# Kernel tuning notes

Measured on AMD Instinct MI355X. Metric: run time of the kernel, lower is better.

Reference implementation:

```python
import jax, jax.numpy as jnp
import numpy as np

EPS = 1e-5

def _layernorm(x, w, b):
    mu = jnp.mean(x, axis=-1, keepdims=True)
    var = jnp.mean(jnp.square(x - mu), axis=-1, keepdims=True)
    return (x - mu) * jax.lax.rsqrt(var + EPS) * w + b

def setup_inputs() -> dict:
    N, C = 768, 128
    key = jax.random.key(0)
    ks = jax.random.split(key, 5)
    s = 0.02
    return {
        "pair": jax.random.normal(ks[0], (N, N, C), jnp.float32),
        "mask": jnp.ones((N,), jnp.float32),
        "ln1_w": jnp.ones((C,), jnp.float32),
        "ln1_b": jnp.zeros((C,), jnp.float32),
        "proj_w": jax.random.normal(ks[1], (2 * C, C), jnp.float32) * s,
        "gate_w": jax.random.normal(ks[2], (2 * C, C), jnp.float32) * s,
        "ln2_w": jnp.ones((C,), jnp.float32),
        "ln2_b": jnp.zeros((C,), jnp.float32),
        "out_w": jax.random.normal(ks[3], (C, C), jnp.float32) * s,
        "gating_w": jax.random.normal(ks[4], (C, C), jnp.float32) * s,
    }

def reference(pair, mask, ln1_w, ln1_b, proj_w, gate_w, ln2_w, ln2_b, out_w, gating_w):
    # pair: [N, N, C]; mask: [N]
    x = _layernorm(pair, ln1_w, ln1_b)            # [N,N,C]
    input_pair = x
    proj = x @ proj_w.T                            # [N,N,2C]
    # torch broadcast mask[None,...] over [2C,N,N] multiplies along the j (last) axis
    proj = proj * mask[None, :, None]
    proj = proj * jax.nn.sigmoid(x @ gate_w.T)     # gated projection
    # torch reshape [2C,N,N]->[C,2,N,N] interleaves channels: a=even, b=odd
    a = proj[..., 0::2]                            # [N,N,C]
    b = proj[..., 1::2]                            # [N,N,C]
    # outgoing: 'cik,cjk->cij' == 'ikc,jkc->ijc' in channels-last
    out = jnp.einsum('ikc,jkc->ijc', a, b)         # [N,N,C]
    out = _layernorm(out, ln2_w, ln2_b)
    out = (out @ out_w.T) * jax.nn.sigmoid(input_pair @ gating_w.T)
    return out
```

## Files before the change

kernel.cpp:

```cpp
#include <hip/hip_runtime.h>
#include <cstdint>
#include <cstddef>

typedef __bf16 bf16;
typedef __bf16 bf16x8 __attribute__((ext_vector_type(8)));
typedef float f32x4 __attribute__((ext_vector_type(4)));

#define MFMA16(A, B, Cc) __builtin_amdgcn_mfma_f32_16x16x32_bf16(A, B, Cc, 0, 0, 0)

constexpr int NN = 768;
constexpr int CC = 128;
constexpr int XP = 152;

__device__ __forceinline__ float bfu_to_f(unsigned short u) {
    return __uint_as_float(((unsigned)u) << 16);
}
__device__ __forceinline__ float sigmoidf_(float x) {
    return 1.f / (1.f + __expf(-x));
}

__global__ void kW(const float* __restrict__ proj_w, const float* __restrict__ gate_w,
                   const float* __restrict__ out_w, const float* __restrict__ gating_w,
                   bf16* __restrict__ wB)
{
    int idx = (blockIdx.x * 256 + threadIdx.x) * 4;
    const float* src; int off;
    if (idx < 32768)      { src = proj_w;   off = idx; }
    else if (idx < 65536) { src = gate_w;   off = idx - 32768; }
    else if (idx < 81920) { src = out_w;    off = idx - 65536; }
    else                  { src = gating_w; off = idx - 81920; }
    float4 v = *(const float4*)(src + off);
    bf16 o[4] = {(bf16)v.x, (bf16)v.y, (bf16)v.z, (bf16)v.w};
    *(uint2*)(wB + idx) = *(const uint2*)o;
}

__global__ __launch_bounds__(256, 2) void kA(
    const float* __restrict__ pair, const float* __restrict__ mask,
    const float* __restrict__ ln1_w, const float* __restrict__ ln1_b,
    const bf16* __restrict__ wB,
    bf16* __restrict__ aT, bf16* __restrict__ bT)
{
    __shared__ bf16 xs[32][XP];
    __shared__ bf16 ob[32][520];

    const int tid  = threadIdx.x;
    const int lane = tid & 63;
    const int wv   = tid >> 6;
    const int r0   = blockIdx.x * 32;
    const int i    = r0 / NN;
    const int k0   = r0 % NN;

    {
        float g0 = ln1_w[lane], g1 = ln1_w[lane + 64];
        float b0 = ln1_b[lane], b1 = ln1_b[lane + 64];
        for (int rr = 0; rr < 8; ++rr) {
            int row = wv * 8 + rr;
            const float* pr = pair + (size_t)(r0 + row) * CC;
            float v0 = pr[lane], v1 = pr[lane + 64];
            float s = v0 + v1, q = v0 * v0 + v1 * v1;
            for (int off = 32; off > 0; off >>= 1) {
                s += __shfl_xor(s, off);
                q += __shfl_xor(q, off);
            }
            float mu   = s * (1.f / 128.f);
            float rstd = rsqrtf(q * (1.f / 128.f) - mu * mu + 1e-5f);
            xs[row][lane]      = (bf16)((v0 - mu) * rstd * g0 + b0);
            xs[row][lane + 64] = (bf16)((v1 - mu) * rstd * g1 + b1);
        }
    }
    __syncthreads();

    {
        const int m = lane & 15, quad = lane >> 4;
        const bf16* wProj = wB;
        const bf16* wGate = wB + 32768;
        f32x4 acc[2][8] = {};
        for (int ks = 0; ks < 4; ++ks) {
            bf16x8 a0 = *(const bf16x8*)&xs[m][ks * 32 + quad * 8];
            bf16x8 a1 = *(const bf16x8*)&xs[m + 16][ks * 32 + quad * 8];
            for (int t = 0; t < 8; ++t) {
                int n0 = wv * 128 + t * 16;
                const bf16* wp = (n0 < 256) ? (wProj + (size_t)n0 * CC)
                                            : (wGate + (size_t)(n0 - 256) * CC);
                bf16x8 bfr = *(const bf16x8*)(wp + (size_t)m * CC + ks * 32 + quad * 8);
                acc[0][t] = MFMA16(a0, bfr, acc[0][t]);
                acc[1][t] = MFMA16(a1, bfr, acc[1][t]);
            }
        }
        for (int t = 0; t < 8; ++t) {
            int n = wv * 128 + t * 16 + m;
            for (int mt = 0; mt < 2; ++mt)
                for (int r = 0; r < 4; ++r)
                    ob[mt * 16 + quad * 4 + r][n] = (bf16)acc[mt][t][r];
        }
    }
    __syncthreads();

    {
        const int isB = tid >> 7;
        const int ch  = tid & 127;
        unsigned packed[16];
        bf16* o = (bf16*)packed;
        for (int mm = 0; mm < 32; ++mm) {
            unsigned pw = *(const unsigned*)&ob[mm][2 * ch];
            unsigned gw = *(const unsigned*)&ob[mm][256 + 2 * ch];
            unsigned short pu = isB ? (unsigned short)(pw >> 16) : (unsigned short)(pw & 0xffffu);
            unsigned short gu = isB ? (unsigned short)(gw >> 16) : (unsigned short)(gw & 0xffffu);
            float p  = bfu_to_f(pu);
            float g  = bfu_to_f(gu);
            float mk = mask[k0 + mm];
            o[mm] = (bf16)(p * mk * sigmoidf_(g));
        }
        bf16* dst = (isB ? bT : aT) + (size_t)ch * NN * NN + (size_t)i * NN + k0;
        for (int qq = 0; qq < 4; ++qq)
            ((uint4*)dst)[qq] = ((const uint4*)packed)[qq];
    }
}

__global__ __launch_bounds__(256, 2) void kB(
    const bf16* __restrict__ aT, const bf16* __restrict__ bT,
    bf16* __restrict__ oT)
{
    __shared__ bf16 As[128 * 32];
    __shared__ bf16 Bs[128 * 32];

    const int tid  = threadIdx.x;
    const int lane = tid & 63;
    const int wv   = tid >> 6;
    const int c    = blockIdx.x / 36;
    const int t    = blockIdx.x % 36;
    const int i0   = (t / 6) * 128, j0 = (t % 6) * 128;
    const bf16* Ab = aT + (size_t)c * NN * NN;
    const bf16* Bb = bT + (size_t)c * NN * NN;
    const int wm = wv & 1, wn = wv >> 1;
    const int m = lane & 15, quad = lane >> 4;

    f32x4 acc[4][4] = {};
    for (int ks = 0; ks < 24; ++ks) {
        const int k0 = ks * 32;
        uint4 av[2], bv[2];
        for (int h = 0; h < 2; ++h) {
            int chunk = h * 256 + tid;
            int row = chunk >> 2, part = chunk & 3;
            av[h] = *(const uint4*)(Ab + (size_t)(i0 + row) * NN + k0 + part * 8);
            bv[h] = *(const uint4*)(Bb + (size_t)(j0 + row) * NN + k0 + part * 8);
        }
        __syncthreads();
        for (int h = 0; h < 2; ++h) {
            int chunk = h * 256 + tid;
            int row = chunk >> 2, part = chunk & 3;
            int slot = part ^ ((row >> 1) & 3);
            *(uint4*)&As[row * 32 + slot * 8] = av[h];
            *(uint4*)&Bs[row * 32 + slot * 8] = bv[h];
        }
        __syncthreads();
        bf16x8 af[4], bf_[4];
        for (int mt = 0; mt < 4; ++mt) {
            int row = wm * 64 + mt * 16 + m;
            int slot = quad ^ ((row >> 1) & 3);
            af[mt] = *(const bf16x8*)&As[row * 32 + slot * 8];
        }
        for (int nt = 0; nt < 4; ++nt) {
            int row = wn * 64 + nt * 16 + m;
            int slot = quad ^ ((row >> 1) & 3);
            bf_[nt] = *(const bf16x8*)&Bs[row * 32 + slot * 8];
        }
        for (int mt = 0; mt < 4; ++mt)
            for (int nt = 0; nt < 4; ++nt)
                acc[mt][nt] = MFMA16(af[mt], bf_[nt], acc[mt][nt]);
    }

    bf16* ob = oT + (size_t)c * NN * NN;
    for (int mt = 0; mt < 4; ++mt)
        for (int nt = 0; nt < 4; ++nt) {
            int row = i0 + wm * 64 + mt * 16 + quad * 4;
            int col = j0 + wn * 64 + nt * 16 + m;
            for (int r = 0; r < 4; ++r)
                ob[(size_t)(row + r) * NN + col] = (bf16)acc[mt][nt][r];
        }
}

__global__ __launch_bounds__(256, 2) void kC(
    const bf16* __restrict__ oT, const float* __restrict__ pair,
    const float* __restrict__ ln1_w, const float* __restrict__ ln1_b,
    const float* __restrict__ ln2_w, const float* __restrict__ ln2_b,
    const bf16* __restrict__ wB, float* __restrict__ out)
{
    __shared__ bf16 x1[32][XP];
    __shared__ bf16 x2[32][XP];

    const int tid  = threadIdx.x;
    const int lane = tid & 63;
    const int wv   = tid >> 6;
    const int r0   = blockIdx.x * 32;
    const int i    = r0 / NN;
    const int j0   = r0 % NN;

    {
        int cch = tid >> 1, jp = (tid & 1) * 16;
        const bf16* src = oT + (size_t)cch * NN * NN + (size_t)i * NN + j0 + jp;
        bf16 v[16];
        *(uint4*)&v[0] = ((const uint4*)src)[0];
        *(uint4*)&v[8] = ((const uint4*)src)[1];
        for (int q = 0; q < 16; ++q) x2[jp + q][cch] = v[q];
    }

    {
        float g0 = ln1_w[lane], g1 = ln1_w[lane + 64];
        float b0 = ln1_b[lane], b1 = ln1_b[lane + 64];
        for (int rr = 0; rr < 8; ++rr) {
            int row = wv * 8 + rr;
            const float* pr = pair + (size_t)(r0 + row) * CC;
            float v0 = pr[lane], v1 = pr[lane + 64];
            float s = v0 + v1, q = v0 * v0 + v1 * v1;
            for (int off = 32; off > 0; off >>= 1) {
                s += __shfl_xor(s, off);
                q += __shfl_xor(q, off);
            }
            float mu   = s * (1.f / 128.f);
            float rstd = rsqrtf(q * (1.f / 128.f) - mu * mu + 1e-5f);
            x1[row][lane]      = (bf16)((v0 - mu) * rstd * g0 + b0);
            x1[row][lane + 64] = (bf16)((v1 - mu) * rstd * g1 + b1);
        }
    }
    __syncthreads();

    {
        float g0 = ln2_w[lane], g1 = ln2_w[lane + 64];
        float b0 = ln2_b[lane], b1 = ln2_b[lane + 64];
        for (int rr = 0; rr < 8; ++rr) {
            int row = wv * 8 + rr;
            float v0 = (float)x2[row][lane], v1 = (float)x2[row][lane + 64];
            float s = v0 + v1, q = v0 * v0 + v1 * v1;
            for (int off = 32; off > 0; off >>= 1) {
                s += __shfl_xor(s, off);
                q += __shfl_xor(q, off);
            }
            float mu   = s * (1.f / 128.f);
            float rstd = rsqrtf(q * (1.f / 128.f) - mu * mu + 1e-5f);
            x2[row][lane]      = (bf16)((v0 - mu) * rstd * g0 + b0);
            x2[row][lane + 64] = (bf16)((v1 - mu) * rstd * g1 + b1);
        }
    }
    __syncthreads();

    const int m = lane & 15, quad = lane >> 4;
    const bf16* wOut  = wB + 65536;
    const bf16* wGat  = wB + 81920;
    f32x4 accy[2][2] = {}, accg[2][2] = {};
    for (int ks = 0; ks < 4; ++ks) {
        bf16x8 a20 = *(const bf16x8*)&x2[m][ks * 32 + quad * 8];
        bf16x8 a21 = *(const bf16x8*)&x2[m + 16][ks * 32 + quad * 8];
        bf16x8 a10 = *(const bf16x8*)&x1[m][ks * 32 + quad * 8];
        bf16x8 a11 = *(const bf16x8*)&x1[m + 16][ks * 32 + quad * 8];
        for (int nt = 0; nt < 2; ++nt) {
            int n0 = wv * 32 + nt * 16;
            bf16x8 bo = *(const bf16x8*)(wOut + (size_t)(n0 + m) * CC + ks * 32 + quad * 8);
            bf16x8 bg = *(const bf16x8*)(wGat + (size_t)(n0 + m) * CC + ks * 32 + quad * 8);
            accy[0][nt] = MFMA16(a20, bo, accy[0][nt]);
            accy[1][nt] = MFMA16(a21, bo, accy[1][nt]);
            accg[0][nt] = MFMA16(a10, bg, accg[0][nt]);
            accg[1][nt] = MFMA16(a11, bg, accg[1][nt]);
        }
    }

    for (int mt = 0; mt < 2; ++mt)
        for (int nt = 0; nt < 2; ++nt) {
            int col = wv * 32 + nt * 16 + m;
            for (int r = 0; r < 4; ++r) {
                size_t off = (size_t)(r0 + mt * 16 + quad * 4 + r) * CC + col;
                out[off] = accy[mt][nt][r] * sigmoidf_(accg[mt][nt][r]);
            }
        }
}

extern "C" void kernel_launch(void* const* d_in, const int* in_sizes, int n_in,
                              void* d_out, int out_size, void* d_ws, size_t ws_size,
                              hipStream_t stream)
{
    const float* pair     = (const float*)d_in[0];
    const float* mask     = (const float*)d_in[1];
    const float* ln1_w    = (const float*)d_in[2];
    const float* ln1_b    = (const float*)d_in[3];
    const float* proj_w   = (const float*)d_in[4];
    const float* gate_w   = (const float*)d_in[5];
    const float* ln2_w    = (const float*)d_in[6];
    const float* ln2_b    = (const float*)d_in[7];
    const float* out_w    = (const float*)d_in[8];
    const float* gating_w = (const float*)d_in[9];
    float* out = (float*)d_out;

    const size_t plane = (size_t)CC * NN * NN;
    bf16* aT = (bf16*)d_ws;
    bf16* bT = aT + plane;
    bf16* oT = bT + plane;
    bf16* wB = oT + plane;

    kW<<<96, 256, 0, stream>>>(proj_w, gate_w, out_w, gating_w, wB);
    kA<<<(NN * NN) / 32, 256, 0, stream>>>(pair, mask, ln1_w, ln1_b, wB, aT, bT);
    kB<<<CC * 36, 256, 0, stream>>>(aT, bT, oT);
    kC<<<(NN * NN) / 32, 256, 0, stream>>>(oT, pair, ln1_w, ln1_b, ln2_w, ln2_b, wB, out);
}
```

Measured before the change: 1.798 ms.

## Prefetch next K tile, remap block order, and stage epilogue stores through LDS

The batched per-channel GEMM kernel now issues global loads for the next K slice into registers before computing on the current one, which overlaps memory latency with the MFMA work. Block indices are remapped so consecutive blocks land on different channels, spreading work across memory channels and caches. The epilogue writes results into swizzled shared memory and then stores full 16-byte rows to global memory, replacing scattered 2-byte stores. This costs extra registers and extra barriers in the epilogue.

Result: faster. 1.710 ms (-4.9%).

```diff
diff --git a/kernel.cpp b/kernel.cpp
--- a/kernel.cpp
+++ b/kernel.cpp
@@ -121,30 +121,36 @@
     const bf16* __restrict__ aT, const bf16* __restrict__ bT,
     bf16* __restrict__ oT)
 {
-    __shared__ bf16 As[128 * 32];
-    __shared__ bf16 Bs[128 * 32];
+    __shared__ __align__(16) bf16 smem[8192];
+    bf16* As = smem;
+    bf16* Bs = smem + 4096;
 
     const int tid  = threadIdx.x;
     const int lane = tid & 63;
     const int wv   = tid >> 6;
-    const int c    = blockIdx.x / 36;
-    const int t    = blockIdx.x % 36;
-    const int i0   = (t / 6) * 128, j0 = (t % 6) * 128;
+
+    const int bid = blockIdx.x;
+    const int w   = (bid & 7) * ((CC * 36) / 8) + (bid >> 3);
+    const int c   = w / 36;
+    const int t   = w % 36;
+    const int i0  = (t / 6) * 128, j0 = (t % 6) * 128;
+
     const bf16* Ab = aT + (size_t)c * NN * NN;
     const bf16* Bb = bT + (size_t)c * NN * NN;
     const int wm = wv & 1, wn = wv >> 1;
     const int m = lane & 15, quad = lane >> 4;
 
     f32x4 acc[4][4] = {};
+    uint4 av[2], bv[2];
+
+    for (int h = 0; h < 2; ++h) {
+        int chunk = h * 256 + tid;
+        int row = chunk >> 2, part = chunk & 3;
+        av[h] = *(const uint4*)(Ab + (size_t)(i0 + row) * NN + part * 8);
+        bv[h] = *(const uint4*)(Bb + (size_t)(j0 + row) * NN + part * 8);
+    }
+
     for (int ks = 0; ks < 24; ++ks) {
-        const int k0 = ks * 32;
-        uint4 av[2], bv[2];
-        for (int h = 0; h < 2; ++h) {
-            int chunk = h * 256 + tid;
-            int row = chunk >> 2, part = chunk & 3;
-            av[h] = *(const uint4*)(Ab + (size_t)(i0 + row) * NN + k0 + part * 8);
-            bv[h] = *(const uint4*)(Bb + (size_t)(j0 + row) * NN + k0 + part * 8);
-        }
         __syncthreads();
         for (int h = 0; h < 2; ++h) {
             int chunk = h * 256 + tid;
@@ -154,6 +160,15 @@
             *(uint4*)&Bs[row * 32 + slot * 8] = bv[h];
         }
         __syncthreads();
+        if (ks < 23) {
+            const int k0 = (ks + 1) * 32;
+            for (int h = 0; h < 2; ++h) {
+                int chunk = h * 256 + tid;
+                int row = chunk >> 2, part = chunk & 3;
+                av[h] = *(const uint4*)(Ab + (size_t)(i0 + row) * NN + k0 + part * 8);
+                bv[h] = *(const uint4*)(Bb + (size_t)(j0 + row) * NN + k0 + part * 8);
+            }
+        }
         bf16x8 af[4], bf_[4];
         for (int mt = 0; mt < 4; ++mt) {
             int row = wm * 64 + mt * 16 + m;
@@ -171,13 +186,28 @@
     }
 
     bf16* ob = oT + (size_t)c * NN * NN;
-    for (int mt = 0; mt < 4; ++mt)
-        for (int nt = 0; nt < 4; ++nt) {
-            int row = i0 + wm * 64 + mt * 16 + quad * 4;
-            int col = j0 + wn * 64 + nt * 16 + m;
-            for (int r = 0; r < 4; ++r)
-                ob[(size_t)(row + r) * NN + col] = (bf16)acc[mt][nt][r];
-        }
+    for (int p = 0; p < 2; ++p) {
+        __syncthreads();
+        if (wm == p) {
+            for (int mt = 0; mt < 4; ++mt)
+                for (int nt = 0; nt < 4; ++nt) {
+                    int rb = mt * 16 + quad * 4;
+                    for (int r = 0; r < 4; ++r) {
+                        int rr = rb + r;
+                        int colb = (wn * 64 + nt * 16 + m) ^ (quad << 4) ^ ((rr & 3) << 3);
+                        smem[rr * 128 + colb] = (bf16)acc[mt][nt][r];
+                    }
+                }
+        }
+        __syncthreads();
+        const int rr = tid >> 2, q = tid & 3;
+        const int swz = (((rr >> 2) & 3) << 4) ^ ((rr & 3) << 3);
+        bf16* dst = ob + (size_t)(i0 + p * 64 + rr) * NN + (j0 + q * 32);
+        for (int cc = 0; cc < 4; ++cc) {
+            int col = (q * 32 + cc * 8) ^ swz;
+            ((uint4*)dst)[cc] = *(const uint4*)&smem[rr * 128 + col];
+        }
+    }
 }
 
 __global__ __launch_bounds__(256, 2) void kC(
```
